# Kernel optimization log

Hardware: AMD Instinct MI355X
Metric: run time of the kernel (lower is better)

## Reference

```python
import jax, jax.numpy as jnp
import numpy as np

EPS = 1e-5

def _bilinear_sample(xb, ys, xs):
    # xb: [C,H,W]; ys, xs: [H,W] float sample coordinates (zero outside bounds)
    C, H, W = xb.shape
    y0 = jnp.floor(ys); x0 = jnp.floor(xs)
    y1 = y0 + 1.0;      x1 = x0 + 1.0
    wy1 = ys - y0; wy0 = 1.0 - wy1
    wx1 = xs - x0; wx0 = 1.0 - wx1
    def g(yi, xi):
        valid = (yi >= 0) & (yi < H) & (xi >= 0) & (xi < W)
        yc = jnp.clip(yi, 0, H - 1).astype(jnp.int32)
        xc = jnp.clip(xi, 0, W - 1).astype(jnp.int32)
        return xb[:, yc, xc] * valid[None].astype(xb.dtype)  # [C,H,W]
    return (g(y0, x0) * (wy0 * wx0)[None] + g(y0, x1) * (wy0 * wx1)[None]
          + g(y1, x0) * (wy1 * wx0)[None] + g(y1, x1) * (wy1 * wx1)[None])

def _deform_conv2d(x, offset, mask, w, b):
    # x:[B,C,H,W] offset:[B,18,H,W] mask:[B,9,H,W] w:[Co,C,3,3] b:[Co]
    B, C, H, W = x.shape
    Co = w.shape[0]
    ii = jnp.arange(H, dtype=x.dtype)[:, None]
    jj = jnp.arange(W, dtype=x.dtype)[None, :]
    cols = []
    for k in range(9):  # fixed 3x3 kernel positions, row-major (dy=offset[2k], dx=offset[2k+1])
        ky, kx = k // 3 - 1, k % 3 - 1
        ys = ii + ky + offset[:, 2 * k]      # [B,H,W]
        xs = jj + kx + offset[:, 2 * k + 1]
        v = jax.vmap(_bilinear_sample)(x, ys, xs)  # [B,C,H,W]
        cols.append(v * mask[:, k][:, None])
    cols = jnp.stack(cols, axis=1)               # [B,9,C,H,W]
    out = jnp.einsum('bkchw,ock->bohw', cols, w.reshape(Co, C, 9))
    return out + b[None, :, None, None]

def setup_inputs() -> dict:
    key = jax.random.key(0)
    k1, k2, k3, k4 = jax.random.split(key, 4)
    B, Cin, Cout, H, W = 8, 64, 64, 128, 128
    x = jax.random.normal(k1, (B, Cin, H, W), dtype=jnp.float32)
    # offset/mask conv: small weights so learned offsets stay O(1) pixels;
    # bias[18:]=2.0 as in the module's init (masks start near sigmoid(2))
    w_off = jax.random.normal(k2, (27, Cin, 3, 3), dtype=jnp.float32) * 0.01
    b_off = jnp.concatenate([jnp.zeros((18,), jnp.float32), jnp.full((9,), 2.0, jnp.float32)])
    w_dcn = jax.random.normal(k3, (Cout, Cin, 3, 3), dtype=jnp.float32) / np.sqrt(Cin * 9)
    b_dcn = jax.random.normal(k4, (Cout,), dtype=jnp.float32) * 0.01
    return {"x": x, "w_off": w_off, "b_off": b_off, "w_dcn": w_dcn, "b_dcn": b_dcn}

def reference(x, w_off, b_off, w_dcn, b_dcn):
    dn = ('NCHW', 'OIHW', 'NCHW')
    om = jax.lax.conv_general_dilated(x, w_off, (1, 1), 'SAME', dimension_numbers=dn)
    om = om + b_off[None, :, None, None]
    offset = om[:, :18]
    mask = jax.nn.sigmoid(om[:, 18:])
    y = _deform_conv2d(x, offset, mask, w_dcn, b_dcn)
    # InstanceNorm2d (affine=False, biased variance) + ReLU
    mu = jnp.mean(y, axis=(2, 3), keepdims=True)
    var = jnp.var(y, axis=(2, 3), keepdims=True)
    y = (y - mu) * jax.lax.rsqrt(var + EPS)
    return jax.nn.relu(y)
```

## Files before the change

kernel.cpp:

```cpp
#include <hip/hip_runtime.h>
#include <hip/hip_fp16.h>

#define BB   8
#define CIN  64
#define COUT 64
#define HH   128
#define WW   128
#define HWSZ (HH * WW)

typedef _Float16 f16x8 __attribute__((ext_vector_type(8)));
typedef _Float16 h2v   __attribute__((ext_vector_type(2)));
typedef float    f32x4 __attribute__((ext_vector_type(4)));

__device__ __forceinline__ unsigned short f2h_u(float f) {
    __half h = __float2half(f);
    return __half_as_ushort(h);
}
__device__ __forceinline__ unsigned duph(float f) {
    unsigned u = (unsigned)f2h_u(f);
    return u | (u << 16);
}

__device__ __forceinline__ unsigned comb2h(unsigned a, unsigned b, unsigned c, unsigned d,
                                           h2v W0, h2v W1, h2v W2, h2v W3) {
    h2v A = *(h2v*)&a, B = *(h2v*)&b, C = *(h2v*)&c, D = *(h2v*)&d;
    h2v r = A * W0;
    r += B * W1;
    r += C * W2;
    r += D * W3;
    return *(unsigned*)&r;
}

__global__ __launch_bounds__(256) void k_tr(const float* __restrict__ x,
                                            const float* __restrict__ wd,
                                            const float* __restrict__ wof,
                                            unsigned short* __restrict__ xT,
                                            unsigned short* __restrict__ wdT,
                                            unsigned short* __restrict__ wofT,
                                            float4* __restrict__ sums4)
{
    const int t = threadIdx.x;
    const int id = blockIdx.x;
    if (id >= 512) {
        if (id == 512) sums4[t] = make_float4(0.f, 0.f, 0.f, 0.f);
        int base = (id - 512) * 256 + t;
#pragma unroll
        for (int j = 0; j < 4; ++j) {
            int idx = base + j * 16384;
            if (idx < 36864) {
                int k = idx >> 12, rem = idx & 4095, co = rem >> 6, c = rem & 63;
                wdT[idx] = f2h_u(wd[(co * 64 + c) * 9 + k]);
            } else if (idx < 55296) {
                int jj = idx - 36864;
                int k = jj >> 11, rem = jj & 2047, o = rem >> 6, c = rem & 63;
                wofT[jj] = (o < 27) ? f2h_u(wof[(o * 64 + c) * 9 + k]) : 0;
            }
        }
        return;
    }
    __shared__ unsigned short tile[256 * 66];
    const int b = id & 7;
    const int p0 = (id >> 3) * 256;
#pragma unroll
    for (int i = 0; i < 16; ++i) {
        int c = i * 4 + (t >> 6);
        int pl = (t & 63) * 4;
        float4 v = *(const float4*)(x + (((size_t)b * 64 + c) << 14) + p0 + pl);
        tile[(pl + 0) * 66 + c] = f2h_u(v.x);
        tile[(pl + 1) * 66 + c] = f2h_u(v.y);
        tile[(pl + 2) * 66 + c] = f2h_u(v.z);
        tile[(pl + 3) * 66 + c] = f2h_u(v.w);
    }
    __syncthreads();
#pragma unroll
    for (int i = 0; i < 8; ++i) {
        int idd = i * 256 + t;
        int pt = idd >> 3, ck = idd & 7;
        const unsigned* srcp = (const unsigned*)&tile[pt * 66 + ck * 8];
        uint4 r;
        r.x = srcp[0]; r.y = srcp[1]; r.z = srcp[2]; r.w = srcp[3];
        *(uint4*)(xT + ((size_t)b << 20) + (size_t)(p0 + pt) * 64 + ck * 8) = r;
    }
}

__global__ __launch_bounds__(256, 2) void k_off(
    const unsigned short* __restrict__ xT, const unsigned short* __restrict__ wofT,
    const float* __restrict__ bof, float* __restrict__ om)
{
    __shared__ unsigned short tile[8 * 521 * 8];
    const int t = threadIdx.x;
    const int lane = t & 63, wv = t >> 6;
    const int q = lane >> 4, l15 = lane & 15;
    const int b = blockIdx.x & 7;
    const int xblk = blockIdx.x >> 3;
    const int h0 = xblk * 2;
    const int r0 = h0 - 1;
    const unsigned short* xb = xT + ((size_t)b << 20);

#pragma unroll
    for (int i = 0; i < 17; ++i) {
        int id = i * 256 + t;
        if (id < 4160) {
            int m = id & 7, lin = id >> 3;
            int row = lin / 130, col = lin % 130;
            int gy = r0 + row, gx = col - 1;
            uint4 v = {0u, 0u, 0u, 0u};
            if (((unsigned)gy < (unsigned)HH) && ((unsigned)gx < (unsigned)WW))
                v = *(const uint4*)(xb + ((size_t)(gy * WW + gx) << 6) + m * 8);
            *(uint4*)&tile[(m * 521 + lin) * 8] = v;
        }
    }
    __syncthreads();

    const int hrow = h0 + (wv >> 1);
    const int c0 = (wv & 1) * 64;

    f32x4 acc[2][4];
#pragma unroll
    for (int mt = 0; mt < 2; ++mt)
#pragma unroll
        for (int nt = 0; nt < 4; ++nt) acc[mt][nt] = (f32x4){0.f, 0.f, 0.f, 0.f};

#pragma unroll
    for (int k = 0; k < 9; ++k) {
        const int ky = k / 3 - 1, kx = k % 3 - 1;
        const int trow = (hrow - h0) + ky + 1;
        const unsigned short* wk = wofT + k * 2048;
#pragma unroll
        for (int ks = 0; ks < 2; ++ks) {
            f16x8 af[2], bfr[4];
#pragma unroll
            for (int mt = 0; mt < 2; ++mt)
                af[mt] = *(const f16x8*)(wk + (mt * 16 + l15) * 64 + ks * 32 + q * 8);
#pragma unroll
            for (int nt = 0; nt < 4; ++nt) {
                int tc = c0 + nt * 16 + l15 + kx + 1;
                bfr[nt] = *(const f16x8*)&tile[((ks * 4 + q) * 521 + trow * 130 + tc) * 8];
            }
#pragma unroll
            for (int mt = 0; mt < 2; ++mt)
#pragma unroll
                for (int nt = 0; nt < 4; ++nt)
                    acc[mt][nt] = __builtin_amdgcn_mfma_f32_16x16x32_f16(
                        af[mt], bfr[nt], acc[mt][nt], 0, 0, 0);
        }
    }

    const int p0 = xblk * 256 + wv * 64;
    float* omb = om + (size_t)b * 27 * HWSZ;
#pragma unroll
    for (int mt = 0; mt < 2; ++mt)
#pragma unroll
        for (int r = 0; r < 4; ++r) {
            int o = mt * 16 + q * 4 + r;
            if (o < 27) {
                float bias = bof[o];
#pragma unroll
                for (int nt = 0; nt < 4; ++nt) {
                    int pp = p0 + nt * 16 + l15;
                    float v = acc[mt][nt][r] + bias;
                    if (o >= 18) v = 1.f / (1.f + __expf(-v));
                    omb[(size_t)o * HWSZ + pp] = v;
                }
            }
        }
}

__global__ __launch_bounds__(256, 2) void k_dcn(
    const unsigned short* __restrict__ xT, const float* __restrict__ om,
    const unsigned short* __restrict__ wdT, const float* __restrict__ bd,
    float* __restrict__ out, float2* __restrict__ sums)
{
    __shared__ unsigned short col_sh[4][64 * 80];
    __shared__ unsigned       adr_sh[4][4][64];
    __shared__ uint4          w_sh[4][64];
    __shared__ float          redS[4][64];
    __shared__ float          redQ[4][64];

    const int t = threadIdx.x;
    const int lane = t & 63, wv = t >> 6;
    const int q = lane >> 4, l15 = lane & 15;
    const int b = blockIdx.x & 7;
    const int pblk = (blockIdx.x >> 3) * 256;
    const int p = pblk + t;
    const int h = p >> 7, w = p & 127;
    const char* xbB = (const char*)(xT + ((size_t)b << 20));
    const float* omp = om + (size_t)b * 27 * HWSZ + p;
    const int gck = lane & 7;

    f32x4 acc[4][4];
#pragma unroll
    for (int mt = 0; mt < 4; ++mt)
#pragma unroll
        for (int nt = 0; nt < 4; ++nt) acc[mt][nt] = (f32x4){0.f, 0.f, 0.f, 0.f};

#define LOADG(P, g) { \
    int pt_ = (g) * 8 + (lane >> 3); \
    unsigned o0_ = adr_sh[wv][0][pt_]; \
    unsigned o1_ = adr_sh[wv][1][pt_]; \
    unsigned o2_ = adr_sh[wv][2][pt_]; \
    unsigned o3_ = adr_sh[wv][3][pt_]; \
    int bo_ = gck * 16; \
    P[0] = *(const uint4*)(xbB + o0_ + bo_); \
    P[1] = *(const uint4*)(xbB + o1_ + bo_); \
    P[2] = *(const uint4*)(xbB + o2_ + bo_); \
    P[3] = *(const uint4*)(xbB + o3_ + bo_); }

#define COMBG(P, g) { \
    int pt_ = (g) * 8 + (lane >> 3); \
    uint4 pw_ = w_sh[wv][pt_]; \
    h2v W0_ = *(h2v*)&pw_.x, W1_ = *(h2v*)&pw_.y; \
    h2v W2_ = *(h2v*)&pw_.z, W3_ = *(h2v*)&pw_.w; \
    uint4 R_; \
    R_.x = comb2h(P[0].x, P[1].x, P[2].x, P[3].x, W0_, W1_, W2_, W3_); \
    R_.y = comb2h(P[0].y, P[1].y, P[2].y, P[3].y, W0_, W1_, W2_, W3_); \
    R_.z = comb2h(P[0].z, P[1].z, P[2].z, P[3].z, W0_, W1_, W2_, W3_); \
    R_.w = comb2h(P[0].w, P[1].w, P[2].w, P[3].w, W0_, W1_, W2_, W3_); \
    *(uint4*)&col_sh[wv][pt_ * 80 + gck * 8] = R_; }

    float offy = omp[0];
    float offx = omp[HWSZ];
    float mk   = omp[18 * HWSZ];

    for (int k = 0; k < 9; ++k) {
        float ys = (float)(h + (k / 3) - 1) + offy;
        float xs = (float)(w + (k % 3) - 1) + offx;
        float fy0 = floorf(ys), fx0 = floorf(xs);
        float wy1 = ys - fy0, wx1 = xs - fx0;
        float wy0 = 1.f - wy1, wx0 = 1.f - wx1;
        int y0 = (int)fy0, x0 = (int)fx0;
        int y1 = y0 + 1, x1 = x0 + 1;
        bool vy0 = (y0 >= 0) && (y0 < HH), vy1 = (y1 >= 0) && (y1 < HH);
        bool vx0 = (x0 >= 0) && (x0 < WW), vx1 = (x1 >= 0) && (x1 < WW);
        int y0c = min(max(y0, 0), HH - 1), y1c = min(max(y1, 0), HH - 1);
        int x0c = min(max(x0, 0), WW - 1), x1c = min(max(x1, 0), WW - 1);
        adr_sh[wv][0][lane] = (unsigned)((y0c * WW + x0c) << 7);
        adr_sh[wv][1][lane] = (unsigned)((y0c * WW + x1c) << 7);
        adr_sh[wv][2][lane] = (unsigned)((y1c * WW + x0c) << 7);
        adr_sh[wv][3][lane] = (unsigned)((y1c * WW + x1c) << 7);
        w_sh[wv][lane] = make_uint4(
            duph((vy0 && vx0) ? mk * wy0 * wx0 : 0.f),
            duph((vy0 && vx1) ? mk * wy0 * wx1 : 0.f),
            duph((vy1 && vx0) ? mk * wy1 * wx0 : 0.f),
            duph((vy1 && vx1) ? mk * wy1 * wx1 : 0.f));
        int kn = (k < 8) ? k + 1 : 8;
        offy = omp[(2 * kn) * HWSZ];
        offx = omp[(2 * kn + 1) * HWSZ];
        mk   = omp[(18 + kn) * HWSZ];
        __builtin_amdgcn_wave_barrier();

        const unsigned short* wk = wdT + k * 4096;
        f16x8 af[2][4];
#pragma unroll
        for (int ks = 0; ks < 2; ++ks)
#pragma unroll
            for (int mt = 0; mt < 4; ++mt)
                af[ks][mt] = *(const f16x8*)(wk + (mt * 16 + l15) * 64 + ks * 32 + q * 8);

        uint4 pb[3][4];
        LOADG(pb[0], 0);
        LOADG(pb[1], 1);
#pragma unroll
        for (int g = 0; g < 8; ++g) {
            if (g + 2 < 8) LOADG(pb[(g + 2) % 3], g + 2);
            COMBG(pb[g % 3], g);
        }
        __builtin_amdgcn_wave_barrier();

#pragma unroll
        for (int ks = 0; ks < 2; ++ks) {
            f16x8 bfr[4];
#pragma unroll
            for (int nt = 0; nt < 4; ++nt)
                bfr[nt] = *(const f16x8*)&col_sh[wv][(nt * 16 + l15) * 80 + ks * 32 + q * 8];
#pragma unroll
            for (int mt = 0; mt < 4; ++mt)
#pragma unroll
                for (int nt = 0; nt < 4; ++nt)
                    acc[mt][nt] = __builtin_amdgcn_mfma_f32_16x16x32_f16(
                        af[ks][mt], bfr[nt], acc[mt][nt], 0, 0, 0);
        }
    }
#undef LOADG
#undef COMBG

    const int p0 = pblk + wv * 64;
    float* outb = out + (size_t)b * COUT * HWSZ;
#pragma unroll
    for (int mt = 0; mt < 4; ++mt)
#pragma unroll
        for (int r = 0; r < 4; ++r) {
            int co = mt * 16 + q * 4 + r;
            float bias = bd[co];
            float s = 0.f, qq = 0.f;
#pragma unroll
            for (int nt = 0; nt < 4; ++nt) {
                float v = acc[mt][nt][r] + bias;
                outb[(size_t)co * HWSZ + p0 + nt * 16 + l15] = v;
                s += v; qq += v * v;
            }
#pragma unroll
            for (int m = 1; m < 16; m <<= 1) {
                s += __shfl_xor(s, m);
                qq += __shfl_xor(qq, m);
            }
            if (l15 == 0) { redS[wv][co] = s; redQ[wv][co] = qq; }
        }
    __syncthreads();
    if (t < 64) {
        float S = redS[0][t] + redS[1][t] + redS[2][t] + redS[3][t];
        float Q = redQ[0][t] + redQ[1][t] + redQ[2][t] + redQ[3][t];
        atomicAdd(&sums[b * 64 + t].x, S);
        atomicAdd(&sums[b * 64 + t].y, Q);
    }
}

__global__ __launch_bounds__(256) void k_norm(float* __restrict__ out,
                                              const float2* __restrict__ sums)
{
    const int id = blockIdx.x;
    const int b = id & 7;
    const int rest = id >> 3;
    const int co = rest >> 4;
    const int off = rest & 15;
    const int bco = b * 64 + co;
    const int i = (bco << 12) + off * 256 + threadIdx.x;
    float2 sq = sums[bco];
    float mu  = sq.x * (1.f / (float)HWSZ);
    float var = sq.y * (1.f / (float)HWSZ) - mu * mu;
    float rstd = rsqrtf(var + 1e-5f);
    float4* o4 = (float4*)out;
    float4 v = o4[i];
    v.x = fmaxf((v.x - mu) * rstd, 0.f);
    v.y = fmaxf((v.y - mu) * rstd, 0.f);
    v.z = fmaxf((v.z - mu) * rstd, 0.f);
    v.w = fmaxf((v.w - mu) * rstd, 0.f);
    o4[i] = v;
}

extern "C" void kernel_launch(void* const* d_in, const int* in_sizes, int n_in,
                              void* d_out, int out_size, void* d_ws, size_t ws_size,
                              hipStream_t stream) {
    const float* x   = (const float*)d_in[0];
    const float* wof = (const float*)d_in[1];
    const float* bof = (const float*)d_in[2];
    const float* wd  = (const float*)d_in[3];
    const float* bd  = (const float*)d_in[4];
    float* out = (float*)d_out;

    char* ws = (char*)d_ws;
    unsigned short* xT   = (unsigned short*)ws;
    float*          om   = (float*)(ws + 16777216);
    unsigned short* wdT  = (unsigned short*)(ws + 30932992);
    unsigned short* wofT = (unsigned short*)(ws + 31006720);
    float2*         sums = (float2*)(ws + 31043584);

    k_tr    <<<576, 256, 0, stream>>>(x, wd, wof, xT, wdT, wofT, (float4*)sums);
    k_off   <<<512, 256, 0, stream>>>(xT, wofT, bof, om);
    k_dcn   <<<512, 256, 0, stream>>>(xT, om, wdT, bd, out, sums);
    k_norm  <<<8192, 256, 0, stream>>>(out, (const float2*)sums);
}
```

Before: 169.4 us.

## Stage six-row input halo in LDS split into channel halves for bilinear gathers

Changes the transposed fp16 input layout to two 32-channel half planes. The deformable conv kernel now stages a 6-row halo tile per channel half in shared memory, and gathers bilinear corners from LDS instead of global memory. Samples whose offsets fall outside the halo use a per-lane global fallback. The channel loop is split into two passes, each recomputing sampling coordinates and adding block syncs. The aim is to cut scattered global/L2 gather traffic, at the cost of repeated coordinate math, a larger LDS footprint and possible occupancy loss.

```diff
diff --git a/kernel.cpp b/kernel.cpp
--- a/kernel.cpp
+++ b/kernel.cpp
@@ -30,6 +30,7 @@
     r += D * W3;
     return *(unsigned*)&r;
 }
+
 
 __global__ __launch_bounds__(256) void k_tr(const float* __restrict__ x,
                                             const float* __restrict__ wd,
@@ -79,7 +80,8 @@
         const unsigned* srcp = (const unsigned*)&tile[pt * 66 + ck * 8];
         uint4 r;
         r.x = srcp[0]; r.y = srcp[1]; r.z = srcp[2]; r.w = srcp[3];
-        *(uint4*)(xT + ((size_t)b << 20) + (size_t)(p0 + pt) * 64 + ck * 8) = r;
+        *(uint4*)(xT + ((size_t)b << 20) + ((size_t)(ck >> 2) << 19)
+                     + (size_t)(p0 + pt) * 32 + (ck & 3) * 8) = r;
     }
 }
 
@@ -106,7 +108,8 @@
             int gy = r0 + row, gx = col - 1;
             uint4 v = {0u, 0u, 0u, 0u};
             if (((unsigned)gy < (unsigned)HH) && ((unsigned)gx < (unsigned)WW))
-                v = *(const uint4*)(xb + ((size_t)(gy * WW + gx) << 6) + m * 8);
+                v = *(const uint4*)(xb + ((size_t)(m >> 2) << 19)
+                                       + (size_t)(gy * WW + gx) * 32 + (m & 3) * 8);
             *(uint4*)&tile[(m * 521 + lin) * 8] = v;
         }
     }
@@ -171,7 +174,8 @@
     const unsigned short* __restrict__ wdT, const float* __restrict__ bd,
     float* __restrict__ out, float2* __restrict__ sums)
 {
-    __shared__ unsigned short col_sh[4][64 * 80];
+    __shared__ unsigned short tile_sh[6 * 128 * 32];
+    __shared__ unsigned short col_sh[4][64 * 40];
     __shared__ unsigned       adr_sh[4][4][64];
     __shared__ uint4          w_sh[4][64];
     __shared__ float          redS[4][64];
@@ -184,9 +188,11 @@
     const int pblk = (blockIdx.x >> 3) * 256;
     const int p = pblk + t;
     const int h = p >> 7, w = p & 127;
-    const char* xbB = (const char*)(xT + ((size_t)b << 20));
+    const int h0 = pblk >> 7;
+    const unsigned short* xbS = xT + ((size_t)b << 20);
     const float* omp = om + (size_t)b * 27 * HWSZ + p;
-    const int gck = lane & 7;
+    const int gpt = lane >> 2;
+    const int gch = (lane & 3) * 8;
 
     f32x4 acc[4][4];
 #pragma unroll
@@ -195,19 +201,14 @@
         for (int nt = 0; nt < 4; ++nt) acc[mt][nt] = (f32x4){0.f, 0.f, 0.f, 0.f};
 
 #define LOADG(P, g) { \
-    int pt_ = (g) * 8 + (lane >> 3); \
-    unsigned o0_ = adr_sh[wv][0][pt_]; \
-    unsigned o1_ = adr_sh[wv][1][pt_]; \
-    unsigned o2_ = adr_sh[wv][2][pt_]; \
-    unsigned o3_ = adr_sh[wv][3][pt_]; \
-    int bo_ = gck * 16; \
-    P[0] = *(const uint4*)(xbB + o0_ + bo_); \
-    P[1] = *(const uint4*)(xbB + o1_ + bo_); \
-    P[2] = *(const uint4*)(xbB + o2_ + bo_); \
-    P[3] = *(const uint4*)(xbB + o3_ + bo_); }
+    int pt_ = (g) * 16 + gpt; \
+    P[0] = *(const uint4*)&tile_sh[(adr_sh[wv][0][pt_] & 0x7fffu) + gch]; \
+    P[1] = *(const uint4*)&tile_sh[(adr_sh[wv][1][pt_] & 0x7fffu) + gch]; \
+    P[2] = *(const uint4*)&tile_sh[(adr_sh[wv][2][pt_] & 0x7fffu) + gch]; \
+    P[3] = *(const uint4*)&tile_sh[(adr_sh[wv][3][pt_] & 0x7fffu) + gch]; }
 
 #define COMBG(P, g) { \
-    int pt_ = (g) * 8 + (lane >> 3); \
+    int pt_ = (g) * 16 + gpt; \
     uint4 pw_ = w_sh[wv][pt_]; \
     h2v W0_ = *(h2v*)&pw_.x, W1_ = *(h2v*)&pw_.y; \
     h2v W2_ = *(h2v*)&pw_.z, W3_ = *(h2v*)&pw_.w; \
@@ -216,69 +217,117 @@
     R_.y = comb2h(P[0].y, P[1].y, P[2].y, P[3].y, W0_, W1_, W2_, W3_); \
     R_.z = comb2h(P[0].z, P[1].z, P[2].z, P[3].z, W0_, W1_, W2_, W3_); \
     R_.w = comb2h(P[0].w, P[1].w, P[2].w, P[3].w, W0_, W1_, W2_, W3_); \
-    *(uint4*)&col_sh[wv][pt_ * 80 + gck * 8] = R_; }
-
-    float offy = omp[0];
-    float offx = omp[HWSZ];
-    float mk   = omp[18 * HWSZ];
-
-    for (int k = 0; k < 9; ++k) {
-        float ys = (float)(h + (k / 3) - 1) + offy;
-        float xs = (float)(w + (k % 3) - 1) + offx;
-        float fy0 = floorf(ys), fx0 = floorf(xs);
-        float wy1 = ys - fy0, wx1 = xs - fx0;
-        float wy0 = 1.f - wy1, wx0 = 1.f - wx1;
-        int y0 = (int)fy0, x0 = (int)fx0;
-        int y1 = y0 + 1, x1 = x0 + 1;
-        bool vy0 = (y0 >= 0) && (y0 < HH), vy1 = (y1 >= 0) && (y1 < HH);
-        bool vx0 = (x0 >= 0) && (x0 < WW), vx1 = (x1 >= 0) && (x1 < WW);
-        int y0c = min(max(y0, 0), HH - 1), y1c = min(max(y1, 0), HH - 1);
-        int x0c = min(max(x0, 0), WW - 1), x1c = min(max(x1, 0), WW - 1);
-        adr_sh[wv][0][lane] = (unsigned)((y0c * WW + x0c) << 7);
-        adr_sh[wv][1][lane] = (unsigned)((y0c * WW + x1c) << 7);
-        adr_sh[wv][2][lane] = (unsigned)((y1c * WW + x0c) << 7);
-        adr_sh[wv][3][lane] = (unsigned)((y1c * WW + x1c) << 7);
-        w_sh[wv][lane] = make_uint4(
-            duph((vy0 && vx0) ? mk * wy0 * wx0 : 0.f),
-            duph((vy0 && vx1) ? mk * wy0 * wx1 : 0.f),
-            duph((vy1 && vx0) ? mk * wy1 * wx0 : 0.f),
-            duph((vy1 && vx1) ? mk * wy1 * wx1 : 0.f));
-        int kn = (k < 8) ? k + 1 : 8;
-        offy = omp[(2 * kn) * HWSZ];
-        offx = omp[(2 * kn + 1) * HWSZ];
-        mk   = omp[(18 + kn) * HWSZ];
-        __builtin_amdgcn_wave_barrier();
-
-        const unsigned short* wk = wdT + k * 4096;
-        f16x8 af[2][4];
-#pragma unroll
-        for (int ks = 0; ks < 2; ++ks)
+    *(uint4*)&col_sh[wv][pt_ * 40 + gch] = R_; }
+
+    for (int hf = 0; hf < 2; ++hf) {
+        __syncthreads();
+        const unsigned short* xbh = xbS + (hf << 19);
+#pragma unroll
+        for (int i = 0; i < 12; ++i) {
+            int idx = i * 256 + t;
+            int s = idx >> 9, u = idx & 511;
+            int y = h0 - 2 + s;
+            y = min(max(y, 0), HH - 1);
+            uint4 v = *(const uint4*)(xbh + (size_t)y * (WW * 32) + u * 8);
+            *(uint4*)&tile_sh[idx * 8] = v;
+        }
+        __syncthreads();
+
+        float offy = omp[0];
+        float offx = omp[HWSZ];
+        float mk   = omp[18 * HWSZ];
+
+        for (int k = 0; k < 9; ++k) {
+            float ys = (float)(h + (k / 3) - 1) + offy;
+            float xs = (float)(w + (k % 3) - 1) + offx;
+            float fy0 = floorf(ys), fx0 = floorf(xs);
+            float wy1 = ys - fy0, wx1 = xs - fx0;
+            float wy0 = 1.f - wy1, wx0 = 1.f - wx1;
+            int y0 = (int)fy0, x0 = (int)fx0;
+            int y1 = y0 + 1, x1 = x0 + 1;
+            bool vy0 = (y0 >= 0) && (y0 < HH), vy1 = (y1 >= 0) && (y1 < HH);
+            bool vx0 = (x0 >= 0) && (x0 < WW), vx1 = (x1 >= 0) && (x1 < WW);
+            int y0c = min(max(y0, 0), HH - 1), y1c = min(max(y1, 0), HH - 1);
+            int x0c = min(max(x0, 0), WW - 1), x1c = min(max(x1, 0), WW - 1);
+            bool ft = (y0c < h0 - 2) || (y1c > h0 + 3);
+            unsigned a0, a1, a2, a3;
+            if (!ft) {
+                int r0s = (y0c - h0 + 2) * (WW * 32);
+                int r1s = (y1c - h0 + 2) * (WW * 32);
+                a0 = (unsigned)(r0s + x0c * 32);
+                a1 = (unsigned)(r0s + x1c * 32);
+                a2 = (unsigned)(r1s + x0c * 32);
+                a3 = (unsigned)(r1s + x1c * 32);
+            } else {
+                unsigned fb = 0x80000000u;
+                a0 = fb | (unsigned)((y0c * WW + x0c) * 32);
+                a1 = fb | (unsigned)((y0c * WW + x1c) * 32);
+                a2 = fb | (unsigned)((y1c * WW + x0c) * 32);
+                a3 = fb | (unsigned)((y1c * WW + x1c) * 32);
+            }
+            adr_sh[wv][0][lane] = a0;
+            adr_sh[wv][1][lane] = a1;
+            adr_sh[wv][2][lane] = a2;
+            adr_sh[wv][3][lane] = a3;
+            uint4 pw = make_uint4(
+                duph((vy0 && vx0) ? mk * wy0 * wx0 : 0.f),
+                duph((vy0 && vx1) ? mk * wy0 * wx1 : 0.f),
+                duph((vy1 && vx0) ? mk * wy1 * wx0 : 0.f),
+                duph((vy1 && vx1) ? mk * wy1 * wx1 : 0.f));
+            w_sh[wv][lane] = pw;
+            int kn = (k < 8) ? k + 1 : 8;
+            offy = omp[(2 * kn) * HWSZ];
+            offx = omp[(2 * kn + 1) * HWSZ];
+            mk   = omp[(18 + kn) * HWSZ];
+            __builtin_amdgcn_wave_barrier();
+
+            uint4 pb[3][4];
+            LOADG(pb[0], 0);
+            LOADG(pb[1], 1);
+#pragma unroll
+            for (int g = 0; g < 4; ++g) {
+                if (g + 2 < 4) LOADG(pb[(g + 2) % 3], g + 2);
+                COMBG(pb[g % 3], g);
+            }
+
+            if (ft) {
+                const unsigned short* c0 = xbh + (y0c * WW + x0c) * 32;
+                const unsigned short* c1 = xbh + (y0c * WW + x1c) * 32;
+                const unsigned short* c2 = xbh + (y1c * WW + x0c) * 32;
+                const unsigned short* c3 = xbh + (y1c * WW + x1c) * 32;
+                h2v W0 = *(h2v*)&pw.x, W1 = *(h2v*)&pw.y;
+                h2v W2 = *(h2v*)&pw.z, W3 = *(h2v*)&pw.w;
+#pragma unroll
+                for (int j = 0; j < 4; ++j) {
+                    uint4 A  = *(const uint4*)(c0 + j * 8);
+                    uint4 Bv = *(const uint4*)(c1 + j * 8);
+                    uint4 Cv = *(const uint4*)(c2 + j * 8);
+                    uint4 Dv = *(const uint4*)(c3 + j * 8);
+                    uint4 R;
+                    R.x = comb2h(A.x, Bv.x, Cv.x, Dv.x, W0, W1, W2, W3);
+                    R.y = comb2h(A.y, Bv.y, Cv.y, Dv.y, W0, W1, W2, W3);
+                    R.z = comb2h(A.z, Bv.z, Cv.z, Dv.z, W0, W1, W2, W3);
+                    R.w = comb2h(A.w, Bv.w, Cv.w, Dv.w, W0, W1, W2, W3);
+                    *(uint4*)&col_sh[wv][lane * 40 + j * 8] = R;
+                }
+            }
+            __builtin_amdgcn_wave_barrier();
+
+            const unsigned short* wk = wdT + k * 4096;
+            f16x8 af_[4];
 #pragma unroll
             for (int mt = 0; mt < 4; ++mt)
-                af[ks][mt] = *(const f16x8*)(wk + (mt * 16 + l15) * 64 + ks * 32 + q * 8);
-
-        uint4 pb[3][4];
-        LOADG(pb[0], 0);
-        LOADG(pb[1], 1);
-#pragma unroll
-        for (int g = 0; g < 8; ++g) {
-            if (g + 2 < 8) LOADG(pb[(g + 2) % 3], g + 2);
-            COMBG(pb[g % 3], g);
-        }
-        __builtin_amdgcn_wave_barrier();
-
-#pragma unroll
-        for (int ks = 0; ks < 2; ++ks) {
+                af_[mt] = *(const f16x8*)(wk + (mt * 16 + l15) * 64 + (hf << 5) + q * 8);
             f16x8 bfr[4];
 #pragma unroll
             for (int nt = 0; nt < 4; ++nt)
-                bfr[nt] = *(const f16x8*)&col_sh[wv][(nt * 16 + l15) * 80 + ks * 32 + q * 8];
+                bfr[nt] = *(const f16x8*)&col_sh[wv][(nt * 16 + l15) * 40 + q * 8];
 #pragma unroll
             for (int mt = 0; mt < 4; ++mt)
 #pragma unroll
                 for (int nt = 0; nt < 4; ++nt)
                     acc[mt][nt] = __builtin_amdgcn_mfma_f32_16x16x32_f16(
-                        af[ks][mt], bfr[nt], acc[mt][nt], 0, 0, 0);
+                        af_[mt], bfr[nt], acc[mt][nt], 0, 0, 0);
         }
     }
 #undef LOADG
```

Result: faster. 158.4 us (-6.5%).
